# Optimization experiments

Measured on AMD Instinct MI355X. Metric: run time of the kernel, lower is better.

## Reference

```python
import jax, jax.numpy as jnp
import numpy as np

H, W = 512, 512          # resized_height, resized_width
R = 2                    # cdist norm order
B, NGT = 4, 64
MAX_DIST = float(np.sqrt(H ** 2 + W ** 2))
EPS = 1e-6


def setup_inputs() -> dict:
    key = jax.random.key(0)
    k1, k2, k3, k4 = jax.random.split(key, 4)
    prob_map = jax.random.uniform(k1, (B, H, W), dtype=jnp.float32)
    # all entries > 0.2 so the torch filter prob_y[prob_y>0.2] keeps every point
    prob_y = 0.2 + 0.79 * jax.random.uniform(k2, (B, NGT), dtype=jnp.float32)
    gt = jax.random.uniform(k3, (B, NGT, 2), dtype=jnp.float32) * jnp.array([H - 1, W - 1], jnp.float32)
    orig_sizes = jax.random.randint(k4, (B, 2), 512, 2048, dtype=jnp.int32)
    return {"prob_map": prob_map, "prob_y": prob_y, "gt": gt, "orig_sizes": orig_sizes}


def _pixel_locations():
    # cartesian([arange(H), arange(W)]) -> (H*W, 2), row-major
    ii, jj = jnp.meshgrid(jnp.arange(H), jnp.arange(W), indexing="ij")
    return jnp.stack([ii, jj], axis=-1).reshape(-1, 2).astype(jnp.float32)


def _ghd(prob_map, prob_y, gt, orig_sizes):
    locs = _pixel_locations()                      # (P, 2), P = H*W
    resized = jnp.array([H, W], jnp.float32)

    def per_batch(pm, py, g, osz):
        nf = osz.astype(jnp.float32) / resized     # (2,) norm factor
        nx = nf * locs                             # (P, 2)
        ny = nf * g                                # (G, 2)
        diff = jnp.abs(nx[:, None, :] - ny[None, :, :])   # (P, G, 2)
        d = jnp.sum(diff ** R, axis=-1) ** (1.0 / R)      # (P, G)
        p = pm.reshape(-1)                         # (P,)
        n_est_pts = jnp.sum(p)
        n_gt_sum = jnp.sum(jnp.where(py > 0.2, py, 0.0))
        weighted = p[:, None] * py[None, :] * d    # p_x * p_y * d
        term_1 = jnp.sum(jnp.min(weighted, axis=1)) / (n_est_pts + EPS)
        dense = (1.0 - p[:, None]) * MAX_DIST + weighted
        term_2 = jnp.sum(jnp.min(dense, axis=0)) / (n_gt_sum + EPS)
        return term_1, term_2

    t1, t2 = jax.vmap(per_batch)(prob_map, prob_y, gt, orig_sizes)
    return t1.mean() + t2.mean()


def reference(prob_map, prob_y, gt, orig_sizes):
    return _ghd(prob_map, prob_y, gt, orig_sizes)
```

## Files before the change

### kernel.cpp

```cpp
#include <hip/hip_runtime.h>
#include <math.h>

#define HH 512
#define WW 512
#define PP (HH * WW)
#define GG 64
#define BB 4
#define THREADS 512
#define TILE 1024
#define NT (PP / TILE)
#define MAX_DIST 724.0773439350246f
#define EPSV 1e-6f
#define BIGF 3.4e38f


__device__ __forceinline__ float rdlane(float v, int l) {
    return __int_as_float(__builtin_amdgcn_readlane(__float_as_int(v), l));
}

__launch_bounds__(THREADS, 8)
__global__ void ghd_main(const float* __restrict__ prob_map,
                         const float* __restrict__ prob_y,
                         const float* __restrict__ gt,
                         const int*   __restrict__ osz,
                         float*       __restrict__ ws) {
    const int t    = blockIdx.x;
    const int b    = blockIdx.y;
    const int tid  = threadIdx.x;
    const int lane = tid & 63;
    const int wave = tid >> 6;

    __shared__ float wmin[8][GG];
    __shared__ float s_t1[8], s_ne[8];

    const float nf0 = (float)osz[2 * b]     * (1.0f / HH);
    const float nf1 = (float)osz[2 * b + 1] * (1.0f / WW);

    const float2 gxy = ((const float2*)gt)[b * GG + lane];
    const float  gx  = nf0 * gxy.x;
    const float  gy  = nf1 * gxy.y;
    const float  py  = prob_y[b * GG + lane];

    const int    seg0 = t * TILE + wave * 128;
    const float2 p2   = ((const float2*)(prob_map + (size_t)b * PP + seg0))[lane];
    const int    pid0 = seg0 + 2 * lane;
    const float  nx0  = nf0 * (float)(pid0 >> 9);
    const float  nx1a = nf1 * (float)(pid0 & (WW - 1));

    const float* __restrict__ gtb = gt     + (size_t)b * GG * 2;
    const float* __restrict__ pyb = prob_y + (size_t)b * GG;

    float ma = BIGF, mb = BIGF;
#pragma unroll
    for (int g = 0; g < GG; ++g) {
        float sgx = gtb[2 * g];
        float sgy = gtb[2 * g + 1];
        float spy = pyb[g];
        float dx  = fmaf(-nf0, sgx, nx0);
        float dx2 = dx * dx;
        float da  = fmaf(-nf1, sgy, nx1a);
        float db  = da + nf1;
        float pq  = spy * spy;
        ma = fminf(ma, pq * fmaf(da, da, dx2));
        mb = fminf(mb, pq * fmaf(db, db, dx2));
    }
    float t1 = p2.x * __builtin_amdgcn_sqrtf(ma) + p2.y * __builtin_amdgcn_sqrtf(mb);
    float ne = p2.x + p2.y;

    const float dxw  = nf0 * (float)(seg0 >> 9) - gx;
    const float dx2w = dxw * dxw;
    const float ny0  = nf1 * (float)(seg0 & (WW - 1)) - gy;
    float gm0 = BIGF, gm1 = BIGF;
#pragma unroll
    for (int k = 0; k < 64; ++k) {
        float qa  = rdlane(p2.x, k);
        float qb  = rdlane(p2.y, k);
        float dya = fmaf((float)(2 * k),     nf1, ny0);
        float dyb = fmaf((float)(2 * k + 1), nf1, ny0);
        float ea  = __builtin_amdgcn_sqrtf(fmaf(dya, dya, dx2w));
        float eb  = __builtin_amdgcn_sqrtf(fmaf(dyb, dyb, dx2w));
        gm0 = fminf(gm0, fmaf(qa, fmaf(py, ea, -MAX_DIST), MAX_DIST));
        gm1 = fminf(gm1, fmaf(qb, fmaf(py, eb, -MAX_DIST), MAX_DIST));
    }
    wmin[wave][lane] = fminf(gm0, gm1);

#pragma unroll
    for (int off = 1; off < 64; off <<= 1) {
        t1 += __shfl_xor(t1, off);
        ne += __shfl_xor(ne, off);
    }
    if (lane == 0) { s_t1[wave] = t1; s_ne[wave] = ne; }
    __syncthreads();

    if (tid == 0) {
        float st = 0.0f, sn = 0.0f;
#pragma unroll
        for (int w = 0; w < 8; ++w) { st += s_t1[w]; sn += s_ne[w]; }
        ws[256  + b * NT + t] = st;
        ws[1280 + b * NT + t] = sn;
    }
    if (tid < GG) {
        float v = wmin[0][tid];
#pragma unroll
        for (int w = 1; w < 8; ++w) v = fminf(v, wmin[w][tid]);
        atomicMin(reinterpret_cast<unsigned*>(ws) + b * GG + tid, __float_as_uint(v));
    }
}

__global__ void ghd_final(const float* __restrict__ prob_y,
                          const float* __restrict__ ws,
                          float*       __restrict__ out) {
    const int tid = threadIdx.x;
    const int b = tid >> 6;
    const int g = tid & 63;

    float mv  = __uint_as_float(reinterpret_cast<const unsigned*>(ws)[b * GG + g]);
    float py  = prob_y[b * GG + g];
    float pyf = (py > 0.2f) ? py : 0.0f;

    float4 tv = ((const float4*)(ws + 256))[b * (NT / 4) + g];
    float4 nv = ((const float4*)(ws + 1280))[b * (NT / 4) + g];
    float t1s = tv.x + tv.y + tv.z + tv.w;
    float nes = nv.x + nv.y + nv.z + nv.w;

#pragma unroll
    for (int off = 1; off < 64; off <<= 1) {
        mv  += __shfl_xor(mv, off);
        pyf += __shfl_xor(pyf, off);
        t1s += __shfl_xor(t1s, off);
        nes += __shfl_xor(nes, off);
    }
    __shared__ float res[4];
    if (g == 0) res[b] = t1s / (nes + EPSV) + mv / (pyf + EPSV);
    __syncthreads();
    if (tid == 0) out[0] = 0.25f * (res[0] + res[1] + res[2] + res[3]);
}

extern "C" void kernel_launch(void* const* d_in, const int* in_sizes, int n_in,
                              void* d_out, int out_size, void* d_ws, size_t ws_size,
                              hipStream_t stream) {
    const float* prob_map = (const float*)d_in[0];
    const float* prob_y   = (const float*)d_in[1];
    const float* gt       = (const float*)d_in[2];
    const int*   osz      = (const int*)d_in[3];
    float* out = (float*)d_out;
    float* ws  = (float*)d_ws;

    hipMemsetAsync(ws, 0x7f, BB * GG * sizeof(unsigned), stream);

    dim3 grid(NT, BB);
    ghd_main<<<grid, THREADS, 0, stream>>>(prob_map, prob_y, gt, osz, ws);
    ghd_final<<<1, 256, 0, stream>>>(prob_y, ws, out);
}
```

Before: 83.99 us.

## Fuse final reduction into main kernel via last-block atomic counter

Removes the separate finalize kernel. Each block now atomically adds its term-1 and point-count partial sums and bumps a completion counter, and the last block to finish computes the scalar output. The inner column loop also replaces the per-iteration FMA offset computation with an incremental add. This trades one kernel launch for an extra memset and global float atomics. It also makes the summation order nondeterministic.

```diff
diff --git a/kernel.cpp b/kernel.cpp
--- a/kernel.cpp
+++ b/kernel.cpp
@@ -9,6 +9,7 @@
 #define THREADS 512
 #define TILE 1024
 #define NT (PP / TILE)
+#define NBLK (NT * BB)
 #define MAX_DIST 724.0773439350246f
 #define EPSV 1e-6f
 #define BIGF 3.4e38f
@@ -23,15 +24,18 @@
                          const float* __restrict__ prob_y,
                          const float* __restrict__ gt,
                          const int*   __restrict__ osz,
-                         float*       __restrict__ ws) {
+                         float*       __restrict__ ws,
+                         float*       __restrict__ out) {
     const int t    = blockIdx.x;
     const int b    = blockIdx.y;
     const int tid  = threadIdx.x;
     const int lane = tid & 63;
     const int wave = tid >> 6;
 
-    __shared__ float wmin[8][GG];
-    __shared__ float s_t1[8], s_ne[8];
+    __shared__ float    wmin[8][GG];
+    __shared__ float    s_t1[8], s_ne[8];
+    __shared__ float    sres[4];
+    __shared__ unsigned s_last;
 
     const float nf0 = (float)osz[2 * b]     * (1.0f / HH);
     const float nf1 = (float)osz[2 * b + 1] * (1.0f / WW);
@@ -69,18 +73,22 @@
 
     const float dxw  = nf0 * (float)(seg0 >> 9) - gx;
     const float dx2w = dxw * dxw;
-    const float ny0  = nf1 * (float)(seg0 & (WW - 1)) - gy;
+    const float negM = -MAX_DIST;
+    const float posM =  MAX_DIST;
+    float dya  = nf1 * (float)(seg0 & (WW - 1)) - gy;
+    float dyb  = dya + nf1;
+    const float step = nf1 + nf1;
     float gm0 = BIGF, gm1 = BIGF;
 #pragma unroll
     for (int k = 0; k < 64; ++k) {
         float qa  = rdlane(p2.x, k);
         float qb  = rdlane(p2.y, k);
-        float dya = fmaf((float)(2 * k),     nf1, ny0);
-        float dyb = fmaf((float)(2 * k + 1), nf1, ny0);
         float ea  = __builtin_amdgcn_sqrtf(fmaf(dya, dya, dx2w));
         float eb  = __builtin_amdgcn_sqrtf(fmaf(dyb, dyb, dx2w));
-        gm0 = fminf(gm0, fmaf(qa, fmaf(py, ea, -MAX_DIST), MAX_DIST));
-        gm1 = fminf(gm1, fmaf(qb, fmaf(py, eb, -MAX_DIST), MAX_DIST));
+        gm0 = fminf(gm0, fmaf(qa, fmaf(py, ea, negM), posM));
+        gm1 = fminf(gm1, fmaf(qb, fmaf(py, eb, negM), posM));
+        dya += step;
+        dyb += step;
     }
     wmin[wave][lane] = fminf(gm0, gm1);
 
@@ -96,44 +104,43 @@
         float st = 0.0f, sn = 0.0f;
 #pragma unroll
         for (int w = 0; w < 8; ++w) { st += s_t1[w]; sn += s_ne[w]; }
-        ws[256  + b * NT + t] = st;
-        ws[1280 + b * NT + t] = sn;
+        atomicAdd(&ws[1 + b], st);
+        atomicAdd(&ws[5 + b], sn);
     }
     if (tid < GG) {
         float v = wmin[0][tid];
 #pragma unroll
         for (int w = 1; w < 8; ++w) v = fminf(v, wmin[w][tid]);
-        atomicMin(reinterpret_cast<unsigned*>(ws) + b * GG + tid, __float_as_uint(v));
+        atomicMin(reinterpret_cast<unsigned*>(ws) + 16 + b * GG + tid, __float_as_uint(v));
     }
-}
 
-__global__ void ghd_final(const float* __restrict__ prob_y,
-                          const float* __restrict__ ws,
-                          float*       __restrict__ out) {
-    const int tid = threadIdx.x;
-    const int b = tid >> 6;
-    const int g = tid & 63;
-
-    float mv  = __uint_as_float(reinterpret_cast<const unsigned*>(ws)[b * GG + g]);
-    float py  = prob_y[b * GG + g];
-    float pyf = (py > 0.2f) ? py : 0.0f;
-
-    float4 tv = ((const float4*)(ws + 256))[b * (NT / 4) + g];
-    float4 nv = ((const float4*)(ws + 1280))[b * (NT / 4) + g];
-    float t1s = tv.x + tv.y + tv.z + tv.w;
-    float nes = nv.x + nv.y + nv.z + nv.w;
-
+    __threadfence();
+    if (tid == 0) {
+        unsigned old = atomicAdd(reinterpret_cast<unsigned*>(ws), 1u);
+        s_last = (old == NBLK - 1) ? 1u : 0u;
+    }
+    __syncthreads();
+    if (s_last) {
+        if (tid < BB * GG) {
+            const int fb = tid >> 6, fg = tid & 63;
+            unsigned* gm = reinterpret_cast<unsigned*>(ws) + 16;
+            float mv  = __uint_as_float(atomicMin(gm + fb * GG + fg, 0x7f7fffffu));
+            float fpy = prob_y[fb * GG + fg];
+            float pyf = (fpy > 0.2f) ? fpy : 0.0f;
 #pragma unroll
-    for (int off = 1; off < 64; off <<= 1) {
-        mv  += __shfl_xor(mv, off);
-        pyf += __shfl_xor(pyf, off);
-        t1s += __shfl_xor(t1s, off);
-        nes += __shfl_xor(nes, off);
+            for (int off = 1; off < 64; off <<= 1) {
+                mv  += __shfl_xor(mv, off);
+                pyf += __shfl_xor(pyf, off);
+            }
+            if (fg == 0) {
+                float t1s = atomicAdd(&ws[1 + fb], 0.0f);
+                float nes = atomicAdd(&ws[5 + fb], 0.0f);
+                sres[fb] = t1s / (nes + EPSV) + mv / (pyf + EPSV);
+            }
+        }
+        __syncthreads();
+        if (tid == 0) out[0] = 0.25f * (sres[0] + sres[1] + sres[2] + sres[3]);
     }
-    __shared__ float res[4];
-    if (g == 0) res[b] = t1s / (nes + EPSV) + mv / (pyf + EPSV);
-    __syncthreads();
-    if (tid == 0) out[0] = 0.25f * (res[0] + res[1] + res[2] + res[3]);
 }
 
 extern "C" void kernel_launch(void* const* d_in, const int* in_sizes, int n_in,
@@ -146,9 +153,9 @@
     float* out = (float*)d_out;
     float* ws  = (float*)d_ws;
 
-    hipMemsetAsync(ws, 0x7f, BB * GG * sizeof(unsigned), stream);
+    hipMemsetAsync(ws, 0, 9 * sizeof(float), stream);
+    hipMemsetAsync(ws + 16, 0x7f, BB * GG * sizeof(unsigned), stream);
 
     dim3 grid(NT, BB);
-    ghd_main<<<grid, THREADS, 0, stream>>>(prob_map, prob_y, gt, osz, ws);
-    ghd_final<<<1, 256, 0, stream>>>(prob_y, ws, out);
+    ghd_main<<<grid, THREADS, 0, stream>>>(prob_map, prob_y, gt, osz, ws, out);
 }
```

New measurement: 196.0 us. +133.4%, slower.
